# Kernel tuning notes

Measured on AMD Instinct MI355X. Metric: run time of the kernel, lower is better.

Reference implementation:

```python
import jax, jax.numpy as jnp
import numpy as np

B, T, C, HID, K, H = 8, 1024, 512, 2048, 31, 4  # batch, time, in_chans, hidden_chans, kernel, wshare


def setup_inputs() -> dict:
    key = jax.random.key(0)
    ks = jax.random.split(key, 8)
    n = lambda k_, sh, sc: jax.random.normal(k_, sh, dtype=jnp.float32) * sc
    return {
        "x": n(ks[0], (B, T, C), 1.0),
        "Wl": n(ks[1], (H * K, C), 0.05),      # linear_weight.weight
        "bl": n(ks[2], (H * K,), 0.01),          # linear_weight.bias
        "bias": n(ks[3], (C,), 0.02),            # self.bias
        "Wc": n(ks[4], (HID, C, K), 0.01),       # pointwise_conv1.weight (O,I,K)
        "bc": n(ks[5], (HID,), 0.01),            # pointwise_conv1.bias
        "W2": n(ks[6], (C, HID), 0.01),          # w_2.weight
        "b2": n(ks[7], (C,), 0.01),              # w_2.bias
    }


def reference(x, Wl, bl, bias, Wc, bc, W2, b2):
    Bq, Tq, Cq = x.shape
    d = Cq // H  # channels per weight-share head
    # dynamic conv logits: (B,T,H,K)
    logits = (x @ Wl.T + bl).reshape(Bq, Tq, H, K)
    # banded positions: output t attends to t + j - (K-1)//2
    offs = jnp.arange(K) - (K - 1) // 2
    pos = jnp.arange(Tq)[:, None] + offs[None, :]          # (T,K)
    valid = (pos >= 0) & (pos < Tq)
    logits = jnp.where(valid[None, :, None, :], logits, -jnp.inf)
    w = jax.nn.softmax(logits, axis=-1)                     # softmax over window (matches banded softmax over T)
    # gather windowed inputs: (B,T,K,H,d)
    xg = x.reshape(Bq, Tq, H, d)[:, jnp.clip(pos, 0, Tq - 1)]
    y = jnp.einsum('bthk,btkhd->bthd', w, xg).reshape(Bq, Tq, Cq)
    # (B,C,T) + bias
    y = y.transpose(0, 2, 1) + bias[None, :, None]
    # pointwise_conv1: Conv1d(C->HID, kernel K, padding 0) -> T' = T-K+1
    z = jax.lax.conv_general_dilated(y, Wc, (1,), 'VALID',
                                     dimension_numbers=('NCH', 'OIH', 'NCH'))
    z = z + bc[None, :, None]
    z = jax.nn.selu(z.transpose(0, 2, 1))                   # (B,T',HID)
    return z @ W2.T + b2                                    # (B,T',C)
```

## Files before the change

### kernel.cpp

```cpp
#include <hip/hip_runtime.h>
#include <hip/hip_bf16.h>

typedef __attribute__((ext_vector_type(8))) short short8;
typedef __attribute__((ext_vector_type(4))) float f32x4;

#define NB 8
#define NT 1024
#define NC 512
#define NHID 2048
#define NK 31
#define NH 4
#define NTP 994
#define MROWS (NB * NTP)
#define TG 4

__device__ __forceinline__ void gload_lds16(const void* g, void* l) {
  __builtin_amdgcn_global_load_lds(
      (const __attribute__((address_space(1))) void*)g,
      (__attribute__((address_space(3))) void*)l, 16, 0, 0);
}

#define BARX()                                  \
  do {                                          \
    __builtin_amdgcn_sched_barrier(0);          \
    __builtin_amdgcn_s_barrier();               \
    __builtin_amdgcn_sched_barrier(0);          \
  } while (0)
#define LGKM0()                                          \
  do {                                                   \
    asm volatile("s_waitcnt lgkmcnt(0)" ::: "memory");   \
    __builtin_amdgcn_sched_barrier(0);                   \
  } while (0)

__global__ __launch_bounds__(256) void prep_wc(const float* __restrict__ Wc,
                                               __hip_bfloat16* __restrict__ Wt) {
  const int blk = blockIdx.x;
  const int cb = blk & 7;
  const int o0 = (blk >> 3) << 3;
  const int c0 = cb << 6;
  const int obig = o0 >> 8;
  const int orb = o0 & 255;
  __shared__ float lds[8 * 64 * NK];
  for (int ol = 0; ol < 8; ++ol) {
    const float* src = Wc + ((size_t)(o0 + ol) * NC + c0) * NK;
    for (int i = threadIdx.x; i < 64 * NK; i += 256) lds[ol * (64 * NK) + i] = src[i];
  }
  __syncthreads();
  for (int i = threadIdx.x; i < NK * 8 * 64; i += 256) {
    const int k = i >> 9;
    const int rem = i & 511;
    const int ol = rem >> 6;
    const int ci = rem & 63;
    Wt[((size_t)((obig * 8 + cb) * NK + k) << 14) + ((orb + ol) << 6) + (ci ^ (ol << 3))] =
        __float2bfloat16(lds[ol * (64 * NK) + ci * NK + k]);
  }
}

__global__ __launch_bounds__(256) void prep_w2(const float* __restrict__ W2,
                                               __hip_bfloat16* __restrict__ W2t) {
  const int i = blockIdx.x * 256 + threadIdx.x;
  if (i < 32 * 512 * 64) {
    const int oi = i & 63;
    const int c = (i >> 6) & 511;
    const int kb = i >> 15;
    const size_t dst = ((size_t)(((c >> 7) * 32 + kb) * 128 + (c & 127)) << 6) +
                       (oi ^ ((c & 7) << 3));
    W2t[dst] = __float2bfloat16(W2[(size_t)c * NHID + (kb << 6) + oi]);
  }
}

__global__ __launch_bounds__(256) void dynconv(const float* __restrict__ x,
                                               const float* __restrict__ Wl,
                                               const float* __restrict__ bl,
                                               const float* __restrict__ bias,
                                               __hip_bfloat16* __restrict__ Y) {
  const int t0 = blockIdx.x * TG;
  const int b = blockIdx.y;
  const int tid = threadIdx.x, lane = tid & 63, w = tid >> 6;
  __shared__ float xt[TG][NC];
  __shared__ float lg[TG][NH * NK];
  __shared__ float wsm[TG][NH][NK];

  for (int i = tid; i < TG * NC; i += 256) {
    const int tg = i >> 9, c = i & 511;
    xt[tg][c] = x[((size_t)b * NT + t0 + tg) * NC + c];
  }
  __syncthreads();

  for (int i = 0; i < 31; ++i) {
    const int id = (i << 2) | w;
    const float* wrow = Wl + (size_t)id * NC + (lane << 3);
    float wv[8];
#pragma unroll
    for (int u = 0; u < 8; ++u) wv[u] = wrow[u];
    const float blv = bl[id];
#pragma unroll
    for (int tg = 0; tg < TG; ++tg) {
      float s = 0.f;
#pragma unroll
      for (int u = 0; u < 8; ++u) s += xt[tg][(lane << 3) + u] * wv[u];
#pragma unroll
      for (int off = 32; off; off >>= 1) s += __shfl_xor(s, off);
      if (lane == 0) lg[tg][id] = s + blv;
    }
  }
  __syncthreads();

  if (tid < TG * NH) {
    const int tg = tid >> 2, h = tid & 3;
    const int t = t0 + tg;
    int jlo = 15 - t; if (jlo < 0) jlo = 0;
    int jhi = 1038 - t; if (jhi > 30) jhi = 30;
    float mx = -1e30f;
    for (int j = jlo; j <= jhi; ++j) mx = fmaxf(mx, lg[tg][h * NK + j]);
    float ssum = 0.f;
    for (int j = 0; j < NK; ++j) {
      const float e = (j >= jlo && j <= jhi) ? __expf(lg[tg][h * NK + j] - mx) : 0.f;
      wsm[tg][h][j] = e;
      ssum += e;
    }
    const float inv = 1.f / ssum;
    for (int j = 0; j < NK; ++j) wsm[tg][h][j] *= inv;
  }
  __syncthreads();

  const int c = tid << 1;
  const int h = c >> 7;
  const float2* x2 = (const float2*)x;
  const float bias0 = bias[c], bias1 = bias[c + 1];
#pragma unroll
  for (int tg = 0; tg < TG; ++tg) {
    const int t = t0 + tg;
    float a0 = 0.f, a1 = 0.f;
#pragma unroll
    for (int j = 0; j < NK; ++j) {
      int pos = t + j - 15;
      pos = pos < 0 ? 0 : (pos > NT - 1 ? NT - 1 : pos);
      const float wgt = wsm[tg][h][j];
      const float2 v = x2[(((size_t)b * NT + pos) << 8) + tid];
      a0 += wgt * v.x;
      a1 += wgt * v.y;
    }
    const int cs = (c & ~63) | ((c & 63) ^ ((t & 7) << 3));
    __hip_bfloat162 hv;
    hv.x = __float2bfloat16(a0 + bias0);
    hv.y = __float2bfloat16(a1 + bias1);
    *(__hip_bfloat162*)(Y + ((size_t)b * NT + t) * NC + cs) = hv;
  }
}

__global__ __launch_bounds__(512, 2) void conv_gemm(const __hip_bfloat16* __restrict__ Y,
                                                    const __hip_bfloat16* __restrict__ Wt,
                                                    const float* __restrict__ bc,
                                                    __hip_bfloat16* __restrict__ Z) {
  const int o0 = blockIdx.x << 8;
  const int t0 = blockIdx.y << 8;
  const int b = blockIdx.z;
  __shared__ __align__(16) __hip_bfloat16 Ys[288 * 64];
  __shared__ __align__(16) __hip_bfloat16 Bsm[3][256 * 64];
  const int tid = threadIdx.x;
  const int lane = tid & 63, wid = tid >> 6;
  const int wr = wid >> 2, wcid = wid & 3;
  const int obig = o0 >> 8;

  f32x4 acc[8][4] = {};

  auto stageY = [&](int cb_) {
    const int c0 = cb_ << 6;
#pragma unroll
    for (int p = 0; p < 5; ++p) {
      const int i = (p << 9) + tid;
      if (i < 2304) {
        int grow = t0 + (i >> 3);
        if (grow > NT - 1) grow = NT - 1;
        gload_lds16(Y + (((size_t)b * NT + grow) << 9) + c0 + ((i & 7) << 3),
                    &Ys[i << 3]);
      }
    }
  };
  auto stageBc = [&](__hip_bfloat16* dst, int s_, int p) {
    const __hip_bfloat16* wb = Wt + (((size_t)(obig * 248 + s_)) << 14);
    const int i = (p << 9) + tid;
    gload_lds16(wb + (i << 3), dst + (i << 3));
  };

  __hip_bfloat16* b0 = Bsm[0];
  __hip_bfloat16* b1 = Bsm[1];
  __hip_bfloat16* b2 = Bsm[2];

  stageY(0);
#pragma unroll
  for (int p = 0; p < 4; ++p) stageBc(b0, 0, p);
#pragma unroll
  for (int p = 0; p < 4; ++p) stageBc(b1, 1, p);

  short8 av[2][4];
  short8 bv[2][2][2];

  const int l15 = lane & 15;
  const int kob = (lane >> 4) << 3;

  for (int cb = 0; cb < 8; ++cb) {
    for (int k = 0; k < NK; ++k) {
      const int s = cb * 31 + k;
      const bool st = (s <= 245);
      if ((k == 0 && s > 0) || s == 247) {
        asm volatile("s_waitcnt vmcnt(0)" ::: "memory");
      } else {
        asm volatile("s_waitcnt vmcnt(4)" ::: "memory");
      }
      BARX();

      if (st) stageBc(b2, s + 2, 0);
#pragma unroll
      for (int kk = 0; kk < 2; ++kk) {
        const int ko = (kk << 5) + kob;
#pragma unroll
        for (int m = 0; m < 4; ++m) {
          const int r2 = (wr << 7) + (m << 4) + l15 + k;
          av[kk][m] = *(const short8*)&Ys[(r2 << 6) + (ko ^ ((r2 & 7) << 3))];
        }
#pragma unroll
        for (int n = 0; n < 2; ++n) {
          const int br = (wcid << 6) + (n << 4) + l15;
          bv[kk][0][n] = *(const short8*)&b0[(br << 6) + (ko ^ ((br & 7) << 3))];
        }
      }
      BARX();
      LGKM0();
      __builtin_amdgcn_s_setprio(1);
#pragma unroll
      for (int kk = 0; kk < 2; ++kk)
#pragma unroll
        for (int m = 0; m < 4; ++m)
#pragma unroll
          for (int n = 0; n < 2; ++n)
            acc[m][n] = __builtin_amdgcn_mfma_f32_16x16x32_bf16(av[kk][m], bv[kk][0][n],
                                                                acc[m][n], 0, 0, 0);
      __builtin_amdgcn_s_setprio(0);
      BARX();

      if (st) stageBc(b2, s + 2, 1);
#pragma unroll
      for (int kk = 0; kk < 2; ++kk) {
        const int ko = (kk << 5) + kob;
#pragma unroll
        for (int n = 0; n < 2; ++n) {
          const int br = (wcid << 6) + 32 + (n << 4) + l15;
          bv[kk][1][n] = *(const short8*)&b0[(br << 6) + (ko ^ ((br & 7) << 3))];
        }
      }
      BARX();
      LGKM0();
      __builtin_amdgcn_s_setprio(1);
#pragma unroll
      for (int kk = 0; kk < 2; ++kk)
#pragma unroll
        for (int m = 0; m < 4; ++m)
#pragma unroll
          for (int n = 0; n < 2; ++n)
            acc[m][2 + n] = __builtin_amdgcn_mfma_f32_16x16x32_bf16(av[kk][m], bv[kk][1][n],
                                                                    acc[m][2 + n], 0, 0, 0);
      __builtin_amdgcn_s_setprio(0);
      BARX();

      if (st) stageBc(b2, s + 2, 2);
#pragma unroll
      for (int kk = 0; kk < 2; ++kk) {
        const int ko = (kk << 5) + kob;
#pragma unroll
        for (int m = 0; m < 4; ++m) {
          const int r2 = (wr << 7) + 64 + (m << 4) + l15 + k;
          av[kk][m] = *(const short8*)&Ys[(r2 << 6) + (ko ^ ((r2 & 7) << 3))];
        }
      }
      BARX();
      LGKM0();
      __builtin_amdgcn_s_setprio(1);
#pragma unroll
      for (int kk = 0; kk < 2; ++kk)
#pragma unroll
        for (int m = 0; m < 4; ++m)
#pragma unroll
          for (int n = 0; n < 2; ++n)
            acc[4 + m][2 + n] = __builtin_amdgcn_mfma_f32_16x16x32_bf16(
                av[kk][m], bv[kk][1][n], acc[4 + m][2 + n], 0, 0, 0);
      __builtin_amdgcn_s_setprio(0);
      BARX();

      if (st) stageBc(b2, s + 2, 3);
      __builtin_amdgcn_s_setprio(1);
#pragma unroll
      for (int kk = 0; kk < 2; ++kk)
#pragma unroll
        for (int m = 0; m < 4; ++m)
#pragma unroll
          for (int n = 0; n < 2; ++n)
            acc[4 + m][n] = __builtin_amdgcn_mfma_f32_16x16x32_bf16(
                av[kk][m], bv[kk][0][n], acc[4 + m][n], 0, 0, 0);
      __builtin_amdgcn_s_setprio(0);
      BARX();

      __hip_bfloat16* tp = b0; b0 = b1; b1 = b2; b2 = tp;
    }
    if (cb < 7) stageY(cb + 1);
  }

  const float kS = 1.0507009873554805f;
  const float kAS = 1.7580993408473766f;
#pragma unroll
  for (int n = 0; n < 4; ++n) {
    const int col = o0 + (wcid << 6) + (n << 4) + (lane & 15);
    const float bcv = bc[col];
#pragma unroll
    for (int m = 0; m < 8; ++m) {
      const int rbase = (wr << 7) + (m << 4) + ((lane >> 4) << 2);
#pragma unroll
      for (int r = 0; r < 4; ++r) {
        const int tp = t0 + rbase + r;
        if (tp < NTP) {
          const float v = acc[m][n][r] + bcv;
          const float s = v > 0.f ? kS * v : kAS * (__expf(v) - 1.f);
          const size_t grow = (size_t)b * NTP + tp;
          const int cs = (col & ~63) | ((col & 63) ^ (((int)(grow & 7)) << 3));
          Z[grow * NHID + cs] = __float2bfloat16(s);
        }
      }
    }
  }
}

__global__ __launch_bounds__(256) void out_gemm(const __hip_bfloat16* __restrict__ Zm,
                                                const __hip_bfloat16* __restrict__ W2t,
                                                const float* __restrict__ b2,
                                                float* __restrict__ Out) {
  const int n0 = blockIdx.x << 7;
  const int m0 = blockIdx.y << 7;
  __shared__ __align__(16) __hip_bfloat16 As[128 * 64];
  __shared__ __align__(16) __hip_bfloat16 Bs[128 * 64];
  const int tid = threadIdx.x;
  const int lane = tid & 63, wid = tid >> 6;
  const int wr = wid >> 1, wc = wid & 1;

  f32x4 acc[4][4] = {};

  for (int kb = 0; kb < 32; ++kb) {
#pragma unroll
    for (int p = 0; p < 4; ++p) {
      const int i = (p << 8) + tid;
      int row = m0 + (i >> 3);
      if (row > MROWS - 1) row = MROWS - 1;
      gload_lds16(Zm + ((size_t)row << 11) + (kb << 6) + ((i & 7) << 3), &As[i << 3]);
    }
    const __hip_bfloat16* wb = W2t + ((size_t)((n0 >> 7) * 32 + kb) << 13);
#pragma unroll
    for (int p = 0; p < 4; ++p) {
      const int i = (p << 8) + tid;
      gload_lds16(wb + (i << 3), &Bs[i << 3]);
    }
    __syncthreads();
#pragma unroll
    for (int kk = 0; kk < 2; ++kk) {
      const int ko = (kk << 5) + ((lane >> 4) << 3);
      short8 av[4], bv[4];
#pragma unroll
      for (int m = 0; m < 4; ++m) {
        const int r = (wr << 6) + (m << 4) + (lane & 15);
        av[m] = *(const short8*)&As[(r << 6) + (ko ^ ((r & 7) << 3))];
      }
#pragma unroll
      for (int n = 0; n < 4; ++n) {
        const int br = (wc << 6) + (n << 4) + (lane & 15);
        bv[n] = *(const short8*)&Bs[(br << 6) + (ko ^ ((br & 7) << 3))];
      }
#pragma unroll
      for (int m = 0; m < 4; ++m)
#pragma unroll
        for (int n = 0; n < 4; ++n)
          acc[m][n] = __builtin_amdgcn_mfma_f32_16x16x32_bf16(av[m], bv[n], acc[m][n], 0, 0, 0);
    }
    __syncthreads();
  }

#pragma unroll
  for (int n = 0; n < 4; ++n) {
    const int col = n0 + (wc << 6) + (n << 4) + (lane & 15);
    const float b2v = b2[col];
#pragma unroll
    for (int m = 0; m < 4; ++m) {
      const int rbase = m0 + (wr << 6) + (m << 4) + ((lane >> 4) << 2);
#pragma unroll
      for (int r = 0; r < 4; ++r) {
        const int row = rbase + r;
        if (row < MROWS) Out[(size_t)row * NC + col] = acc[m][n][r] + b2v;
      }
    }
  }
}

extern "C" void kernel_launch(void* const* d_in, const int* in_sizes, int n_in,
                              void* d_out, int out_size, void* d_ws, size_t ws_size,
                              hipStream_t stream) {
  const float* x = (const float*)d_in[0];
  const float* Wl = (const float*)d_in[1];
  const float* bl = (const float*)d_in[2];
  const float* bias = (const float*)d_in[3];
  const float* Wc = (const float*)d_in[4];
  const float* bc = (const float*)d_in[5];
  const float* W2 = (const float*)d_in[6];
  const float* b2 = (const float*)d_in[7];
  float* out = (float*)d_out;

  char* ws = (char*)d_ws;
  __hip_bfloat16* Wt = (__hip_bfloat16*)(ws);
  __hip_bfloat16* Y = (__hip_bfloat16*)(ws + 65011712);
  __hip_bfloat16* W2t = (__hip_bfloat16*)(ws + 73400320);
  __hip_bfloat16* Z = (__hip_bfloat16*)(ws + 75497472);

  hipLaunchKernelGGL(prep_wc, dim3(2048), dim3(256), 0, stream, Wc, Wt);
  hipLaunchKernelGGL(prep_w2, dim3(4096), dim3(256), 0, stream, W2, W2t);
  hipLaunchKernelGGL(dynconv, dim3(NT / TG, NB), dim3(256), 0, stream, x, Wl, bl, bias, Y);
  hipLaunchKernelGGL(conv_gemm, dim3(NHID / 256, 4, NB), dim3(512), 0, stream, Y, Wt, bc, Z);
  hipLaunchKernelGGL(out_gemm, dim3(NC / 128, (MROWS + 127) / 128), dim3(256), 0, stream,
                     Z, W2t, b2, out);
}
```

Measured before the change: 711.6 us.

## Collapse per-step barriers into one and use partial LDS waits in conv GEMM

Restructures the conv1 MFMA main loop so each k-step has a single workgroup barrier instead of about eight. All B fragments and the first A fragments are loaded up front. Counted lgkmcnt waits (4, 8, 0) let the MFMAs start while later LDS reads are still in flight. B-fragment swizzled offsets are precomputed outside the loop, and the Y restage now gets an explicit barrier before it. This cuts synchronisation stalls and address arithmetic, at the cost of more live VGPRs for fragments and reliance on the triple-buffer order for correctness.

```diff
diff --git a/kernel.cpp b/kernel.cpp
--- a/kernel.cpp
+++ b/kernel.cpp
@@ -20,16 +20,24 @@
       (__attribute__((address_space(3))) void*)l, 16, 0, 0);
 }
 
-#define BARX()                                  \
+#define FENCE() __builtin_amdgcn_sched_barrier(0)
+#define SBAR()                                  \
   do {                                          \
-    __builtin_amdgcn_sched_barrier(0);          \
+    FENCE();                                    \
     __builtin_amdgcn_s_barrier();               \
-    __builtin_amdgcn_sched_barrier(0);          \
+    FENCE();                                    \
   } while (0)
-#define LGKM0()                                          \
-  do {                                                   \
-    asm volatile("s_waitcnt lgkmcnt(0)" ::: "memory");   \
-    __builtin_amdgcn_sched_barrier(0);                   \
+#define WLGKM(n)                                                 \
+  do {                                                           \
+    FENCE();                                                     \
+    asm volatile("s_waitcnt lgkmcnt(" #n ")" ::: "memory");      \
+    FENCE();                                                     \
+  } while (0)
+#define WVM(n)                                                   \
+  do {                                                           \
+    FENCE();                                                     \
+    asm volatile("s_waitcnt vmcnt(" #n ")" ::: "memory");        \
+    FENCE();                                                     \
   } while (0)
 
 __global__ __launch_bounds__(256) void prep_wc(const float* __restrict__ Wc,
@@ -194,116 +202,121 @@
 #pragma unroll
   for (int p = 0; p < 4; ++p) stageBc(b1, 1, p);
 
-  short8 av[2][4];
-  short8 bv[2][2][2];
-
   const int l15 = lane & 15;
   const int kob = (lane >> 4) << 3;
+  const int R0 = (wr << 7) + l15;
+  const int bkey = (l15 & 7) << 3;
+
+  int boff[2][2][2];
+#pragma unroll
+  for (int kk = 0; kk < 2; ++kk)
+#pragma unroll
+    for (int hf = 0; hf < 2; ++hf)
+#pragma unroll
+      for (int n = 0; n < 2; ++n) {
+        const int br = (wcid << 6) + (hf << 5) + (n << 4) + l15;
+        boff[kk][hf][n] = (br << 6) + (((kk << 5) | kob) ^ bkey);
+      }
 
   for (int cb = 0; cb < 8; ++cb) {
     for (int k = 0; k < NK; ++k) {
       const int s = cb * 31 + k;
       const bool st = (s <= 245);
-      if ((k == 0 && s > 0) || s == 247) {
-        asm volatile("s_waitcnt vmcnt(0)" ::: "memory");
-      } else {
-        asm volatile("s_waitcnt vmcnt(4)" ::: "memory");
-      }
-      BARX();
-
+
+      if ((k == 0 && cb > 0) || s == 247) { WVM(0); } else { WVM(4); }
+      SBAR();
+
+      const int keyv = ((l15 + k) & 7) << 3;
+      const int ako0 = kob ^ keyv;
+      const int ako1 = (32 | kob) ^ keyv;
+      const int arow = (R0 + k) << 6;
+
+      short8 av0[4], av1[4], a20[4], a21[4];
+      short8 bl0[2], bl1[2], bh0[2], bh1[2];
+
+#pragma unroll
+      for (int m = 0; m < 4; ++m) {
+        av0[m] = *(const short8*)&Ys[arow + (m << 10) + ako0];
+        av1[m] = *(const short8*)&Ys[arow + (m << 10) + ako1];
+      }
+#pragma unroll
+      for (int n = 0; n < 2; ++n) {
+        bl0[n] = *(const short8*)&b0[boff[0][0][n]];
+        bl1[n] = *(const short8*)&b0[boff[1][0][n]];
+        bh0[n] = *(const short8*)&b0[boff[0][1][n]];
+        bh1[n] = *(const short8*)&b0[boff[1][1][n]];
+      }
       if (st) stageBc(b2, s + 2, 0);
-#pragma unroll
-      for (int kk = 0; kk < 2; ++kk) {
-        const int ko = (kk << 5) + kob;
-#pragma unroll
-        for (int m = 0; m < 4; ++m) {
-          const int r2 = (wr << 7) + (m << 4) + l15 + k;
-          av[kk][m] = *(const short8*)&Ys[(r2 << 6) + (ko ^ ((r2 & 7) << 3))];
-        }
-#pragma unroll
-        for (int n = 0; n < 2; ++n) {
-          const int br = (wcid << 6) + (n << 4) + l15;
-          bv[kk][0][n] = *(const short8*)&b0[(br << 6) + (ko ^ ((br & 7) << 3))];
-        }
-      }
-      BARX();
-      LGKM0();
+
+      WLGKM(4);
       __builtin_amdgcn_s_setprio(1);
 #pragma unroll
-      for (int kk = 0; kk < 2; ++kk)
-#pragma unroll
-        for (int m = 0; m < 4; ++m)
-#pragma unroll
-          for (int n = 0; n < 2; ++n)
-            acc[m][n] = __builtin_amdgcn_mfma_f32_16x16x32_bf16(av[kk][m], bv[kk][0][n],
-                                                                acc[m][n], 0, 0, 0);
+      for (int m = 0; m < 4; ++m)
+#pragma unroll
+        for (int n = 0; n < 2; ++n)
+          acc[m][n] = __builtin_amdgcn_mfma_f32_16x16x32_bf16(av0[m], bl0[n], acc[m][n], 0, 0, 0);
+#pragma unroll
+      for (int m = 0; m < 4; ++m)
+#pragma unroll
+        for (int n = 0; n < 2; ++n)
+          acc[m][n] = __builtin_amdgcn_mfma_f32_16x16x32_bf16(av1[m], bl1[n], acc[m][n], 0, 0, 0);
       __builtin_amdgcn_s_setprio(0);
-      BARX();
 
       if (st) stageBc(b2, s + 2, 1);
 #pragma unroll
-      for (int kk = 0; kk < 2; ++kk) {
-        const int ko = (kk << 5) + kob;
-#pragma unroll
-        for (int n = 0; n < 2; ++n) {
-          const int br = (wcid << 6) + 32 + (n << 4) + l15;
-          bv[kk][1][n] = *(const short8*)&b0[(br << 6) + (ko ^ ((br & 7) << 3))];
-        }
-      }
-      BARX();
-      LGKM0();
+      for (int m = 0; m < 4; ++m) {
+        a20[m] = *(const short8*)&Ys[arow + 4096 + (m << 10) + ako0];
+        a21[m] = *(const short8*)&Ys[arow + 4096 + (m << 10) + ako1];
+      }
+
+      WLGKM(8);
       __builtin_amdgcn_s_setprio(1);
 #pragma unroll
-      for (int kk = 0; kk < 2; ++kk)
-#pragma unroll
-        for (int m = 0; m < 4; ++m)
-#pragma unroll
-          for (int n = 0; n < 2; ++n)
-            acc[m][2 + n] = __builtin_amdgcn_mfma_f32_16x16x32_bf16(av[kk][m], bv[kk][1][n],
-                                                                    acc[m][2 + n], 0, 0, 0);
+      for (int m = 0; m < 4; ++m)
+#pragma unroll
+        for (int n = 0; n < 2; ++n)
+          acc[m][2 + n] = __builtin_amdgcn_mfma_f32_16x16x32_bf16(av0[m], bh0[n], acc[m][2 + n], 0, 0, 0);
+#pragma unroll
+      for (int m = 0; m < 4; ++m)
+#pragma unroll
+        for (int n = 0; n < 2; ++n)
+          acc[m][2 + n] = __builtin_amdgcn_mfma_f32_16x16x32_bf16(av1[m], bh1[n], acc[m][2 + n], 0, 0, 0);
       __builtin_amdgcn_s_setprio(0);
-      BARX();
 
       if (st) stageBc(b2, s + 2, 2);
-#pragma unroll
-      for (int kk = 0; kk < 2; ++kk) {
-        const int ko = (kk << 5) + kob;
-#pragma unroll
-        for (int m = 0; m < 4; ++m) {
-          const int r2 = (wr << 7) + 64 + (m << 4) + l15 + k;
-          av[kk][m] = *(const short8*)&Ys[(r2 << 6) + (ko ^ ((r2 & 7) << 3))];
-        }
-      }
-      BARX();
-      LGKM0();
+
+      WLGKM(0);
       __builtin_amdgcn_s_setprio(1);
 #pragma unroll
-      for (int kk = 0; kk < 2; ++kk)
-#pragma unroll
-        for (int m = 0; m < 4; ++m)
-#pragma unroll
-          for (int n = 0; n < 2; ++n)
-            acc[4 + m][2 + n] = __builtin_amdgcn_mfma_f32_16x16x32_bf16(
-                av[kk][m], bv[kk][1][n], acc[4 + m][2 + n], 0, 0, 0);
+      for (int m = 0; m < 4; ++m)
+#pragma unroll
+        for (int n = 0; n < 2; ++n)
+          acc[4 + m][2 + n] = __builtin_amdgcn_mfma_f32_16x16x32_bf16(a20[m], bh0[n], acc[4 + m][2 + n], 0, 0, 0);
+#pragma unroll
+      for (int m = 0; m < 4; ++m)
+#pragma unroll
+        for (int n = 0; n < 2; ++n)
+          acc[4 + m][2 + n] = __builtin_amdgcn_mfma_f32_16x16x32_bf16(a21[m], bh1[n], acc[4 + m][2 + n], 0, 0, 0);
+#pragma unroll
+      for (int m = 0; m < 4; ++m)
+#pragma unroll
+        for (int n = 0; n < 2; ++n)
+          acc[4 + m][n] = __builtin_amdgcn_mfma_f32_16x16x32_bf16(a20[m], bl0[n], acc[4 + m][n], 0, 0, 0);
+#pragma unroll
+      for (int m = 0; m < 4; ++m)
+#pragma unroll
+        for (int n = 0; n < 2; ++n)
+          acc[4 + m][n] = __builtin_amdgcn_mfma_f32_16x16x32_bf16(a21[m], bl1[n], acc[4 + m][n], 0, 0, 0);
       __builtin_amdgcn_s_setprio(0);
-      BARX();
 
       if (st) stageBc(b2, s + 2, 3);
-      __builtin_amdgcn_s_setprio(1);
-#pragma unroll
-      for (int kk = 0; kk < 2; ++kk)
-#pragma unroll
-        for (int m = 0; m < 4; ++m)
-#pragma unroll
-          for (int n = 0; n < 2; ++n)
-            acc[4 + m][n] = __builtin_amdgcn_mfma_f32_16x16x32_bf16(
-                av[kk][m], bv[kk][0][n], acc[4 + m][n], 0, 0, 0);
-      __builtin_amdgcn_s_setprio(0);
-      BARX();
 
       __hip_bfloat16* tp = b0; b0 = b1; b1 = b2; b2 = tp;
     }
-    if (cb < 7) stageY(cb + 1);
+    if (cb < 7) {
+      SBAR();
+      stageY(cb + 1);
+    }
   }
 
   const float kS = 1.0507009873554805f;
```

New measurement: 645.2 us. -9.3%, faster.
